# Performance work log

Measured on AMD Instinct MI355X. Metric: run time of the kernel, lower is better.

The kernel has to match this reference:

```python
import jax, jax.numpy as jnp
import numpy as np

D = 256; FF = 1024; NH = 8; NL = 4; NP = 4; DH = D // NH
SHAPES = [(64, 64), (32, 32), (16, 16), (8, 8)]
B = 4; N = sum(h * w for h, w in SHAPES)


def _ln(x, g, b, eps=1e-5):
    m = jnp.mean(x, -1, keepdims=True)
    v = jnp.var(x, -1, keepdims=True)
    return (x - m) * jax.lax.rsqrt(v + eps) * g + b


def _bilinear(v, x, y, H, W):
    # v: [B, H*W, nh, dh]; x, y: [B, Nq, nh, P] pixel coords (grid_sample, align_corners=False, zero pad)
    x0 = jnp.floor(x); y0 = jnp.floor(y)
    fx = x - x0; fy = y - y0
    x0 = x0.astype(jnp.int32); y0 = y0.astype(jnp.int32)
    dh = v.shape[-1]
    acc = 0.0
    for xi, yi, w in ((x0, y0, (1 - fx) * (1 - fy)),
                      (x0 + 1, y0, fx * (1 - fy)),
                      (x0, y0 + 1, (1 - fx) * fy),
                      (x0 + 1, y0 + 1, fx * fy)):
        valid = ((xi >= 0) & (xi < W) & (yi >= 0) & (yi < H)).astype(v.dtype)
        idx = jnp.clip(yi, 0, H - 1) * W + jnp.clip(xi, 0, W - 1)  # [B,Nq,nh,P]
        Bq, Nq, nh, P = idx.shape
        idx2 = idx.transpose(0, 1, 3, 2).reshape(Bq, Nq * P, nh, 1)
        idx2 = jnp.broadcast_to(idx2, (Bq, Nq * P, nh, dh))
        g = jnp.take_along_axis(v, idx2, axis=1)  # [B, Nq*P, nh, dh]
        g = g.reshape(Bq, Nq, P, nh, dh).transpose(0, 1, 3, 2, 4)  # [B,Nq,nh,P,dh]
        acc = acc + g * (w * valid)[..., None]
    return acc


def _msdeform(value, loc, attn, shapes):
    # value [B,N,nh,dh]; loc [B,Nq,nh,L,P,2] in [0,1]; attn [B,Nq,nh,L,P]
    out = 0.0; start = 0
    for l, (H, W) in enumerate(shapes):
        v = value[:, start:start + H * W]
        start += H * W
        x = loc[:, :, :, l, :, 0] * W - 0.5
        y = loc[:, :, :, l, :, 1] * H - 0.5
        s = _bilinear(v, x, y, H, W)  # [B,Nq,nh,P,dh]
        out = out + jnp.einsum('bqhpd,bqhp->bqhd', s, attn[:, :, :, l, :])
    return out


def _forward(src, pos, reference_points, w_value, b_value, w_off, b_off, w_attn, b_attn,
             w_out, b_out, g1, be1, w1, b1, w2, b2, g2, be2, padding_mask, shapes):
    q = src + pos
    value = src @ w_value.T + b_value
    value = jnp.where(padding_mask[..., None], 0.0, value).reshape(B, N, NH, DH)
    off = (q @ w_off.T + b_off).reshape(B, N, NH, NL, NP, 2)
    attn = jax.nn.softmax((q @ w_attn.T + b_attn).reshape(B, N, NH, NL * NP), axis=-1)
    attn = attn.reshape(B, N, NH, NL, NP)
    normalizer = jnp.array([[w, h] for h, w in shapes], jnp.float32)  # [L,2] as (W,H)
    loc = reference_points[:, :, None, :, None, :] + off / normalizer[None, None, None, :, None, :]
    a = _msdeform(value, loc, attn, shapes).reshape(B, N, D) @ w_out.T + b_out
    x = _ln(src + a, g1, be1)
    f = jax.nn.relu(x @ w1.T + b1) @ w2.T + b2
    return _ln(x + f, g2, be2)


def setup_inputs() -> dict:
    key = jax.random.key(0)
    ks = iter(jax.random.split(key, 24))
    def p(shape, scale=0.02):
        return jax.random.normal(next(ks), shape, jnp.float32) * scale
    d = {}
    d['src'] = jax.random.normal(next(ks), (B, N, D), jnp.float32)
    d['pos'] = jax.random.normal(next(ks), (B, N, D), jnp.float32)
    d['reference_points'] = jax.random.uniform(next(ks), (B, N, NL, 2), dtype=jnp.float32)
    d['w_value'] = p((D, D)); d['b_value'] = jnp.zeros((D,), jnp.float32)
    d['w_off'] = p((NH * NL * NP * 2, D), 0.001); d['b_off'] = p((NH * NL * NP * 2,), 0.1)
    d['w_attn'] = p((NH * NL * NP, D)); d['b_attn'] = jnp.zeros((NH * NL * NP,), jnp.float32)
    d['w_out'] = p((D, D)); d['b_out'] = jnp.zeros((D,), jnp.float32)
    d['g1'] = jnp.ones((D,), jnp.float32); d['be1'] = jnp.zeros((D,), jnp.float32)
    d['w1'] = p((FF, D)); d['b1'] = jnp.zeros((FF,), jnp.float32)
    d['w2'] = p((D, FF)); d['b2'] = jnp.zeros((D,), jnp.float32)
    d['g2'] = jnp.ones((D,), jnp.float32); d['be2'] = jnp.zeros((D,), jnp.float32)
    d['spatial_shapes'] = jnp.array(SHAPES, jnp.int32)
    d['level_start_index'] = jnp.array(np.cumsum([0] + [h * w for h, w in SHAPES[:-1]]), jnp.int32)
    d['padding_mask'] = jnp.zeros((B, N), bool)
    return d


def reference(src, pos, reference_points, w_value, b_value, w_off, b_off, w_attn, b_attn,
              w_out, b_out, g1, be1, w1, b1, w2, b2, g2, be2,
              spatial_shapes, level_start_index, padding_mask):
    shapes = [tuple(map(int, s)) for s in np.asarray(spatial_shapes)]  # static per-level shapes
    return _forward(src, pos, reference_points, w_value, b_value, w_off, b_off, w_attn, b_attn,
                    w_out, b_out, g1, be1, w1, b1, w2, b2, g2, be2, padding_mask, shapes)
```

## Files before the change

### kernel.cpp

```cpp
#include <hip/hip_runtime.h>

#define B_SZ   4
#define NTOK   5440
#define MTOT   (B_SZ*NTOK)
#define DMODEL 256
#define FFDIM  1024
#define NROWP  (MTOT/128)

typedef __attribute__((ext_vector_type(8))) __bf16 bf16x8;
typedef __attribute__((ext_vector_type(4))) float  f32x4;

static __device__ __forceinline__ unsigned short f2b(float f) {
    unsigned u = __builtin_bit_cast(unsigned, f);
    u = (u + 0x7FFF + ((u >> 16) & 1)) >> 16;
    return (unsigned short)u;
}
static __device__ __forceinline__ float b2f(unsigned short s) {
    return __builtin_bit_cast(float, (unsigned)s << 16);
}
static __device__ __forceinline__ float lo_bf(unsigned u) {
    return __builtin_bit_cast(float, u << 16);
}
static __device__ __forceinline__ float hi_bf(unsigned u) {
    return __builtin_bit_cast(float, u & 0xffff0000u);
}

#define GLL(gp, lp) __builtin_amdgcn_global_load_lds( \
    (const __attribute__((address_space(1))) void*)(gp), \
    (__attribute__((address_space(3))) void*)(lp), 16, 0, 0)

__global__ __launch_bounds__(256)
void qkv_gemm(const unsigned short* __restrict__ src_bf,
              const unsigned short* __restrict__ q_bf,
              const unsigned short* __restrict__ wv_b,
              const unsigned short* __restrict__ woa_b,
              const float* __restrict__ b_value,
              const float* __restrict__ b_off, const float* __restrict__ b_attn,
              const unsigned char* __restrict__ rowmask,
              unsigned short* __restrict__ value_b, unsigned short* __restrict__ oa_b)
{
    const int K = 256;
    const int id  = blockIdx.x;
    const int xcd = id & 7;
    const int j   = id >> 3;
    const int c   = j % 5;
    const int r   = 8 * (j / 5) + xcd;
    if (r >= NROWP) return;
    const int row0 = r * 128;
    const bool isv = (c < 2);
    const unsigned short* A  = isv ? src_bf : q_bf;
    const unsigned short* Wt = isv ? wv_b : woa_b;
    unsigned short* C = isv ? value_b : oa_b;
    const int ldc  = isv ? 256 : 384;
    const int col0 = (isv ? c : (c - 2)) * 128;

    __shared__ unsigned short As[2][128 * 32];
    __shared__ unsigned short Bs[2][128 * 32];
    const int tid  = threadIdx.x;
    const int lane = tid & 63;
    const int wave = tid >> 6;
    const int wr = (wave >> 1) * 64, wc = (wave & 1) * 64;
    const int mrow = lane & 15, quad = lane >> 4;

    f32x4 acc[4][4] = {};
    const int ri0 = tid >> 2,            ki0 = (tid & 3) * 8;
    const int ri1 = (256 + tid) >> 2,    ki1 = ((256 + tid) & 3) * 8;
    const int lds0 = (wave * 64) * 8, lds1 = (256 + wave * 64) * 8;

    for (int k0 = 0; k0 < K; k0 += 64) {
        __syncthreads();
        #pragma unroll
        for (int s = 0; s < 2; ++s) {
            const int kk = k0 + s * 32;
            GLL(A  + (size_t)(row0 + ri0) * K + kk + ki0, &As[s][lds0]);
            GLL(Wt + (size_t)(col0 + ri0) * K + kk + ki0, &Bs[s][lds0]);
            GLL(A  + (size_t)(row0 + ri1) * K + kk + ki1, &As[s][lds1]);
            GLL(Wt + (size_t)(col0 + ri1) * K + kk + ki1, &Bs[s][lds1]);
        }
        __syncthreads();
        #pragma unroll
        for (int s = 0; s < 2; ++s) {
            bf16x8 af[4], bfr[4];
            #pragma unroll
            for (int t4 = 0; t4 < 4; ++t4) {
                af[t4]  = *(const bf16x8*)&As[s][(wr + t4 * 16 + mrow) * 32 + quad * 8];
                bfr[t4] = *(const bf16x8*)&Bs[s][(wc + t4 * 16 + mrow) * 32 + quad * 8];
            }
            #pragma unroll
            for (int ti = 0; ti < 4; ++ti)
                #pragma unroll
                for (int tj = 0; tj < 4; ++tj)
                    acc[ti][tj] = __builtin_amdgcn_mfma_f32_16x16x32_bf16(
                                      bfr[tj], af[ti], acc[ti][tj], 0, 0, 0);
        }
    }

    #pragma unroll
    for (int ti = 0; ti < 4; ++ti) {
        const int row = row0 + wr + ti * 16 + mrow;
        const bool msk = isv && rowmask[row];
        #pragma unroll
        for (int tj = 0; tj < 4; ++tj) {
            const int col = col0 + wc + tj * 16 + quad * 4;
            const float4 bv = isv ? *(const float4*)(b_value + col)
                            : (col < 256 ? *(const float4*)(b_off + col)
                                         : *(const float4*)(b_attn + col - 256));
            ushort4 o;
            o.x = msk ? 0 : f2b(acc[ti][tj][0] + bv.x);
            o.y = msk ? 0 : f2b(acc[ti][tj][1] + bv.y);
            o.z = msk ? 0 : f2b(acc[ti][tj][2] + bv.z);
            o.w = msk ? 0 : f2b(acc[ti][tj][3] + bv.w);
            *(ushort4*)(C + (size_t)row * ldc + col) = o;
        }
    }
}

__global__ __launch_bounds__(256)
void mfma_gemm(const unsigned short* __restrict__ A,
               const unsigned short* __restrict__ Wt,
               const float* __restrict__ bias,
               unsigned short* __restrict__ Cb,
               int Nout, int K)
{
    const int id  = blockIdx.x;
    const int xcd = id & 7;
    const int j   = id >> 3;
    const int ncol = Nout / 128;
    const int c   = j % ncol;
    const int r   = 8 * (j / ncol) + xcd;
    if (r >= NROWP) return;
    const int row0 = r * 128, col0 = c * 128;

    __shared__ unsigned short As[2][128 * 32];
    __shared__ unsigned short Bs[2][128 * 32];
    const int tid  = threadIdx.x;
    const int lane = tid & 63;
    const int wave = tid >> 6;
    const int wr = (wave >> 1) * 64, wc = (wave & 1) * 64;
    const int mrow = lane & 15, quad = lane >> 4;

    f32x4 acc[4][4] = {};
    const int ri0 = tid >> 2,            ki0 = (tid & 3) * 8;
    const int ri1 = (256 + tid) >> 2,    ki1 = ((256 + tid) & 3) * 8;
    const int lds0 = (wave * 64) * 8, lds1 = (256 + wave * 64) * 8;

    for (int k0 = 0; k0 < K; k0 += 64) {
        __syncthreads();
        #pragma unroll
        for (int s = 0; s < 2; ++s) {
            const int kk = k0 + s * 32;
            GLL(A  + (size_t)(row0 + ri0) * K + kk + ki0, &As[s][lds0]);
            GLL(Wt + (size_t)(col0 + ri0) * K + kk + ki0, &Bs[s][lds0]);
            GLL(A  + (size_t)(row0 + ri1) * K + kk + ki1, &As[s][lds1]);
            GLL(Wt + (size_t)(col0 + ri1) * K + kk + ki1, &Bs[s][lds1]);
        }
        __syncthreads();
        #pragma unroll
        for (int s = 0; s < 2; ++s) {
            bf16x8 af[4], bfr[4];
            #pragma unroll
            for (int t4 = 0; t4 < 4; ++t4) {
                af[t4]  = *(const bf16x8*)&As[s][(wr + t4 * 16 + mrow) * 32 + quad * 8];
                bfr[t4] = *(const bf16x8*)&Bs[s][(wc + t4 * 16 + mrow) * 32 + quad * 8];
            }
            #pragma unroll
            for (int ti = 0; ti < 4; ++ti)
                #pragma unroll
                for (int tj = 0; tj < 4; ++tj)
                    acc[ti][tj] = __builtin_amdgcn_mfma_f32_16x16x32_bf16(
                                      bfr[tj], af[ti], acc[ti][tj], 0, 0, 0);
        }
    }

    #pragma unroll
    for (int ti = 0; ti < 4; ++ti) {
        const int row = row0 + wr + ti * 16 + mrow;
        #pragma unroll
        for (int tj = 0; tj < 4; ++tj) {
            const int col = col0 + wc + tj * 16 + quad * 4;
            const float4 bv = *(const float4*)(bias + col);
            ushort4 o;
            o.x = f2b(fmaxf(acc[ti][tj][0] + bv.x, 0.f));
            o.y = f2b(fmaxf(acc[ti][tj][1] + bv.y, 0.f));
            o.z = f2b(fmaxf(acc[ti][tj][2] + bv.z, 0.f));
            o.w = f2b(fmaxf(acc[ti][tj][3] + bv.w, 0.f));
            *(ushort4*)(Cb + (size_t)row * Nout + col) = o;
        }
    }
}

__global__ __launch_bounds__(256)
void gemm_n64(const unsigned short* __restrict__ A,
              const unsigned short* __restrict__ Wt,
              const float* __restrict__ bias,
              unsigned short* __restrict__ Cb,
              int K)
{
    const int id  = blockIdx.x;
    const int xcd = id & 7;
    const int j   = id >> 3;
    const int c   = j % 4;
    const int r   = 8 * (j / 4) + xcd;
    if (r >= NROWP) return;
    const int row0 = r * 128, col0 = c * 64;

    __shared__ unsigned short As[2][128 * 32];
    __shared__ unsigned short Bs[2][64 * 32];
    const int tid  = threadIdx.x;
    const int lane = tid & 63;
    const int wave = tid >> 6;
    const int wr = wave * 32;
    const int mrow = lane & 15, quad = lane >> 4;

    f32x4 acc[2][4] = {};
    const int ri0 = tid >> 2,            ki0 = (tid & 3) * 8;
    const int ri1 = (256 + tid) >> 2,    ki1 = ((256 + tid) & 3) * 8;
    const int ldsA0 = (wave * 64) * 8, ldsA1 = (256 + wave * 64) * 8;
    const int ldsB  = (wave * 64) * 8;

    for (int k0 = 0; k0 < K; k0 += 64) {
        __syncthreads();
        #pragma unroll
        for (int s = 0; s < 2; ++s) {
            const int kk = k0 + s * 32;
            GLL(A  + (size_t)(row0 + ri0) * K + kk + ki0, &As[s][ldsA0]);
            GLL(A  + (size_t)(row0 + ri1) * K + kk + ki1, &As[s][ldsA1]);
            GLL(Wt + (size_t)(col0 + ri0) * K + kk + ki0, &Bs[s][ldsB]);
        }
        __syncthreads();
        #pragma unroll
        for (int s = 0; s < 2; ++s) {
            bf16x8 af[2], bfr[4];
            #pragma unroll
            for (int ti = 0; ti < 2; ++ti)
                af[ti] = *(const bf16x8*)&As[s][(wr + ti * 16 + mrow) * 32 + quad * 8];
            #pragma unroll
            for (int tj = 0; tj < 4; ++tj)
                bfr[tj] = *(const bf16x8*)&Bs[s][(tj * 16 + mrow) * 32 + quad * 8];
            #pragma unroll
            for (int ti = 0; ti < 2; ++ti)
                #pragma unroll
                for (int tj = 0; tj < 4; ++tj)
                    acc[ti][tj] = __builtin_amdgcn_mfma_f32_16x16x32_bf16(
                                      bfr[tj], af[ti], acc[ti][tj], 0, 0, 0);
        }
    }

    #pragma unroll
    for (int ti = 0; ti < 2; ++ti) {
        const int row = row0 + wr + ti * 16 + mrow;
        #pragma unroll
        for (int tj = 0; tj < 4; ++tj) {
            const int col = col0 + tj * 16 + quad * 4;
            const float4 bv = *(const float4*)(bias + col);
            ushort4 o;
            o.x = f2b(acc[ti][tj][0] + bv.x);
            o.y = f2b(acc[ti][tj][1] + bv.y);
            o.z = f2b(acc[ti][tj][2] + bv.z);
            o.w = f2b(acc[ti][tj][3] + bv.w);
            *(ushort4*)(Cb + (size_t)row * 256 + col) = o;
        }
    }
}

__global__ __launch_bounds__(256)
void addln_kernel(const unsigned short* __restrict__ c,
                  const float* __restrict__ resid_f,
                  const unsigned short* __restrict__ resid_b,
                  const float* __restrict__ g, const float* __restrict__ be,
                  float* __restrict__ out_f, unsigned short* __restrict__ out_b)
{
    const int wave = threadIdx.x >> 6;
    const int lane = threadIdx.x & 63;
    const int row  = blockIdx.x * 4 + wave;
    const size_t base = (size_t)row * 256 + (lane << 2);

    const ushort4 cu = *(const ushort4*)(c + base);
    float4 v;
    v.x = b2f(cu.x); v.y = b2f(cu.y); v.z = b2f(cu.z); v.w = b2f(cu.w);
    if (resid_f) {
        const float4 r = *(const float4*)(resid_f + base);
        v.x += r.x; v.y += r.y; v.z += r.z; v.w += r.w;
    } else {
        const ushort4 r = *(const ushort4*)(resid_b + base);
        v.x += b2f(r.x); v.y += b2f(r.y); v.z += b2f(r.z); v.w += b2f(r.w);
    }

    float s  = v.x + v.y + v.z + v.w;
    float ss = v.x * v.x + v.y * v.y + v.z * v.z + v.w * v.w;
    #pragma unroll
    for (int off = 32; off; off >>= 1) {
        s  += __shfl_xor(s, off, 64);
        ss += __shfl_xor(ss, off, 64);
    }
    const float mean = s * (1.f / 256.f);
    const float var  = ss * (1.f / 256.f) - mean * mean;
    const float rstd = rsqrtf(var + 1e-5f);

    const float4 gv = *(const float4*)(g  + (lane << 2));
    const float4 bv = *(const float4*)(be + (lane << 2));
    float4 o;
    o.x = (v.x - mean) * rstd * gv.x + bv.x;
    o.y = (v.y - mean) * rstd * gv.y + bv.y;
    o.z = (v.z - mean) * rstd * gv.z + bv.z;
    o.w = (v.w - mean) * rstd * gv.w + bv.w;
    if (out_f) *(float4*)(out_f + base) = o;
    if (out_b) {
        ushort4 u; u.x = f2b(o.x); u.y = f2b(o.y); u.z = f2b(o.z); u.w = f2b(o.w);
        *(ushort4*)(out_b + base) = u;
    }
}

__global__ __launch_bounds__(256)
void sampling_kernel(const unsigned short* __restrict__ value,
                     const unsigned short* __restrict__ oa,
                     const float* __restrict__ refp,
                     unsigned short* __restrict__ samp)
{
    __shared__ unsigned s_pk[64 * 68];
    const int t0  = blockIdx.x * 8;
    const int tid = threadIdx.x;

    #pragma unroll
    for (int rep = 0; rep < 4; ++rep) {
        const int e   = rep * 256 + tid;
        const int tok = e >> 7;
        const int hp  = e & 127;
        const int h   = hp >> 4, i16 = hp & 15, l = i16 >> 2;
        const int t   = t0 + tok;

        const float ex = __expf(b2f(oa[(size_t)t * 384 + 256 + h * 16 + i16]));
        float ssum = ex;
        #pragma unroll
        for (int o = 8; o; o >>= 1) ssum += __shfl_xor(ssum, o, 16);
        const float aw = ex / ssum;

        const int   Wl_t[4]  = {64, 32, 16, 8};
        const int   LST_t[4] = {0, 4096, 5120, 5376};
        const int   Wl  = Wl_t[l];
        const int   LST = LST_t[l];
        const float fW  = (float)Wl;

        const unsigned ov = *(const unsigned*)&oa[(size_t)t * 384 + h * 32 + i16 * 2];
        const float ox = lo_bf(ov), oy = hi_bf(ov);
        const float2 rxy = *(const float2*)&refp[(size_t)t * 8 + l * 2];
        const float x = rxy.x * fW + ox - 0.5f;
        const float y = rxy.y * fW + oy - 0.5f;
        const float x0 = floorf(x), y0 = floorf(y);
        const float fx = x - x0, fy = y - y0;
        const int   ix = (int)x0, iy = (int)y0;
        const bool  vx0 = (ix >= 0) & (ix < Wl), vx1 = (ix + 1 >= 0) & (ix + 1 < Wl);

        const int base = (tok * 8 + h) * 68 + i16 * 4;
        #pragma unroll
        for (int j = 0; j < 2; ++j) {
            const int  yv = iy + j;
            const bool vy = (yv >= 0) & (yv < Wl);
            const float wy = (j ? fy : 1.f - fy) * aw;
            const int  rowi = LST + yv * Wl;
            const float w0 = (vy & vx0) ? wy * (1.f - fx) : 0.f;
            const float w1 = (vy & vx1) ? wy * fx : 0.f;
            const unsigned i0 = (vy & vx0) ? (unsigned)(rowi + ix) : 0u;
            const unsigned i1 = (vy & vx1) ? (unsigned)(rowi + ix + 1) : 0u;
            s_pk[base + j * 2 + 0] = (i0 << 16) | f2b(w0);
            s_pk[base + j * 2 + 1] = (i1 << 16) | f2b(w1);
        }
    }
    __syncthreads();

    const int wv_  = tid >> 6;
    const int lane = tid & 63;
    const int t2   = lane >> 5;
    const int h    = (lane >> 2) & 7;
    const int dq   = lane & 3;
    const int tok  = wv_ * 2 + t2;
    const int t    = t0 + tok;
    const int b    = t / NTOK;
    const char* vb = (const char*)value + ((size_t)b * NTOK * 256 + h * 32 + dq * 8) * 2;
    const unsigned* sp = s_pk + (tok * 8 + h) * 68;

    float a0 = 0.f, a1 = 0.f, a2 = 0.f, a3 = 0.f;
    float a4 = 0.f, a5 = 0.f, a6 = 0.f, a7 = 0.f;

    unsigned pkc = sp[0];
    uint4 vc = *(const uint4*)(vb + (size_t)(pkc >> 16) * 512);
    #pragma unroll 8
    for (int i = 0; i < 64; ++i) {
        unsigned pkn = 0; uint4 vn = make_uint4(0, 0, 0, 0);
        if (i < 63) {
            pkn = sp[i + 1];
            vn = *(const uint4*)(vb + (size_t)(pkn >> 16) * 512);
        }
        const float w = lo_bf(pkc);
        a0 += lo_bf(vc.x) * w; a1 += hi_bf(vc.x) * w;
        a2 += lo_bf(vc.y) * w; a3 += hi_bf(vc.y) * w;
        a4 += lo_bf(vc.z) * w; a5 += hi_bf(vc.z) * w;
        a6 += lo_bf(vc.w) * w; a7 += hi_bf(vc.w) * w;
        pkc = pkn; vc = vn;
    }
    ushort4 o0, o1;
    o0.x = f2b(a0); o0.y = f2b(a1); o0.z = f2b(a2); o0.w = f2b(a3);
    o1.x = f2b(a4); o1.y = f2b(a5); o1.z = f2b(a6); o1.w = f2b(a7);
    unsigned short* op = samp + (size_t)t * 256 + h * 32 + dq * 8;
    *(ushort4*)(op)     = o0;
    *(ushort4*)(op + 4) = o1;
}

__global__ __launch_bounds__(256)
void prep_kernel(const float* __restrict__ src, const float* __restrict__ pos,
                 const float* __restrict__ wv, const float* __restrict__ woff,
                 const float* __restrict__ wattn, const float* __restrict__ wout,
                 const float* __restrict__ w1, const float* __restrict__ w2,
                 unsigned short* __restrict__ q_bf, unsigned short* __restrict__ src_bf,
                 unsigned short* __restrict__ wv_b, unsigned short* __restrict__ woa_b,
                 unsigned short* __restrict__ wout_b,
                 unsigned short* __restrict__ w1_b, unsigned short* __restrict__ w2_b)
{
    const int v = blockIdx.x * 256 + threadIdx.x;
    if (v < 1392640) {
        const float4 s = ((const float4*)src)[v];
        const float4 p = ((const float4*)pos)[v];
        ushort4 qo, so;
        qo.x = f2b(s.x + p.x); qo.y = f2b(s.y + p.y);
        qo.z = f2b(s.z + p.z); qo.w = f2b(s.w + p.w);
        so.x = f2b(s.x); so.y = f2b(s.y); so.z = f2b(s.z); so.w = f2b(s.w);
        ((ushort4*)q_bf)[v]   = qo;
        ((ushort4*)src_bf)[v] = so;
        return;
    }
    const int v2 = v - 1392640;
    const float* s; unsigned short* d; int off;
    if      (v2 <  16384) { s = wv;    d = wv_b;          off = v2; }
    else if (v2 <  32768) { s = woff;  d = woa_b;         off = v2 - 16384; }
    else if (v2 <  40960) { s = wattn; d = woa_b + 65536; off = v2 - 32768; }
    else if (v2 <  57344) { s = wout;  d = wout_b;        off = v2 - 40960; }
    else if (v2 < 122880) { s = w1;    d = w1_b;          off = v2 - 57344; }
    else                  { s = w2;    d = w2_b;          off = v2 - 122880; }
    const float4 f = ((const float4*)s)[off];
    ushort4 u; u.x = f2b(f.x); u.y = f2b(f.y); u.z = f2b(f.z); u.w = f2b(f.w);
    ((ushort4*)d)[off] = u;
}

extern "C" void kernel_launch(void* const* d_in, const int* in_sizes, int n_in,
                              void* d_out, int out_size, void* d_ws, size_t ws_size,
                              hipStream_t stream) {
    const float* src     = (const float*)d_in[0];
    const float* pos     = (const float*)d_in[1];
    const float* refp    = (const float*)d_in[2];
    const float* w_value = (const float*)d_in[3];
    const float* b_value = (const float*)d_in[4];
    const float* w_off   = (const float*)d_in[5];
    const float* b_off   = (const float*)d_in[6];
    const float* w_attn  = (const float*)d_in[7];
    const float* b_attn  = (const float*)d_in[8];
    const float* w_out   = (const float*)d_in[9];
    const float* b_out   = (const float*)d_in[10];
    const float* g1      = (const float*)d_in[11];
    const float* be1     = (const float*)d_in[12];
    const float* w1      = (const float*)d_in[13];
    const float* b1      = (const float*)d_in[14];
    const float* w2      = (const float*)d_in[15];
    const float* b2      = (const float*)d_in[16];
    const float* g2      = (const float*)d_in[17];
    const float* be2     = (const float*)d_in[18];
    const unsigned char* pmask = (const unsigned char*)d_in[21];

    char* ws = (char*)d_ws;
    const size_t SZ16 = (size_t)MTOT * 256 * 2;
    unsigned short* q_bf    = (unsigned short*)(ws);
    unsigned short* src_bf  = (unsigned short*)(ws + SZ16);
    unsigned short* value_b = (unsigned short*)(ws + 2 * SZ16);
    unsigned short* oa_b    = (unsigned short*)(ws + 3 * SZ16);
    unsigned short* samp    = (unsigned short*)(ws + 3 * SZ16 + SZ16 * 3 / 2);
    unsigned short* h_bf    = (unsigned short*)(ws + 5 * SZ16 + SZ16 * 3 / 2);
    unsigned short* wts     = (unsigned short*)(ws + 9 * SZ16 + SZ16 * 3 / 2);
    unsigned short* C1_bf   = (unsigned short*)(ws + 2 * SZ16);
    unsigned short* x_bf    = (unsigned short*)(ws);
    unsigned short* C2_bf   = samp;

    unsigned short* wv_b    = wts;
    unsigned short* woa_b   = wv_b   + 65536;
    unsigned short* wout_b  = woa_b  + 98304;
    unsigned short* w1_b    = wout_b + 65536;
    unsigned short* w2_b    = w1_b   + 262144;

    const dim3 blk(256);

    prep_kernel<<<dim3(6176), blk, 0, stream>>>(src, pos, w_value, w_off, w_attn,
                                                w_out, w1, w2, q_bf, src_bf,
                                                wv_b, woa_b, wout_b, w1_b, w2_b);
    qkv_gemm<<<dim3(8 * 5 * 22), blk, 0, stream>>>(
        src_bf, q_bf, wv_b, woa_b, b_value, b_off, b_attn, pmask, value_b, oa_b);
    sampling_kernel<<<dim3(MTOT / 8), blk, 0, stream>>>(value_b, oa_b, refp, samp);
    gemm_n64<<<dim3(8 * 4 * 22), blk, 0, stream>>>(
        samp, wout_b, b_out, C1_bf, DMODEL);
    addln_kernel<<<dim3(MTOT / 4), blk, 0, stream>>>(
        C1_bf, src, nullptr, g1, be1, nullptr, x_bf);
    mfma_gemm<<<dim3(8 * 8 * 22), blk, 0, stream>>>(
        x_bf, w1_b, b1, h_bf, FFDIM, DMODEL);
    gemm_n64<<<dim3(8 * 4 * 22), blk, 0, stream>>>(
        h_bf, w2_b, b2, C2_bf, FFDIM);
    addln_kernel<<<dim3(MTOT / 4), blk, 0, stream>>>(
        C2_bf, nullptr, x_bf, g2, be2, (float*)d_out, nullptr);
}
```

Measured before the change: 273.7 us.

## Software-pipeline GEMM K-loops with explicit waitcnts and batch sampling gathers

The three GEMM kernels now prefetch the next 32-wide K slice into the free LDS buffer while MFMAs run on the current one. Raw s_waitcnt and s_barrier calls replace the paired __syncthreads, and K is made a compile-time constant so the loops fully unroll. The sampling kernel issues eight independent value gathers before accumulating them, which raises memory-level parallelism at the cost of more registers. The workspace buffers are also remapped, which risks aliasing mistakes if the fixed offsets overlap live data.

```diff
diff --git a/kernel.cpp b/kernel.cpp
--- a/kernel.cpp
+++ b/kernel.cpp
@@ -28,6 +28,10 @@
 #define GLL(gp, lp) __builtin_amdgcn_global_load_lds( \
     (const __attribute__((address_space(1))) void*)(gp), \
     (__attribute__((address_space(3))) void*)(lp), 16, 0, 0)
+
+#define WAITVM(n)  __builtin_amdgcn_s_waitcnt(0x0F70 | (n))
+#define WAITLGKM0  __builtin_amdgcn_s_waitcnt(0xC07F)
+#define BAR        __builtin_amdgcn_s_barrier()
 
 __global__ __launch_bounds__(256)
 void qkv_gemm(const unsigned short* __restrict__ src_bf,
@@ -62,37 +66,46 @@
     const int wr = (wave >> 1) * 64, wc = (wave & 1) * 64;
     const int mrow = lane & 15, quad = lane >> 4;
 
+    const int ri0 = tid >> 2,         ki0 = (tid & 3) * 8;
+    const int ri1 = (256 + tid) >> 2, ki1 = ((256 + tid) & 3) * 8;
+    const int lds0 = (wave * 64) * 8, lds1 = (256 + wave * 64) * 8;
+
+    const unsigned short* Ar0 = A  + (size_t)(row0 + ri0) * K + ki0;
+    const unsigned short* Br0 = Wt + (size_t)(col0 + ri0) * K + ki0;
+    const unsigned short* Ar1 = A  + (size_t)(row0 + ri1) * K + ki1;
+    const unsigned short* Br1 = Wt + (size_t)(col0 + ri1) * K + ki1;
+
     f32x4 acc[4][4] = {};
-    const int ri0 = tid >> 2,            ki0 = (tid & 3) * 8;
-    const int ri1 = (256 + tid) >> 2,    ki1 = ((256 + tid) & 3) * 8;
-    const int lds0 = (wave * 64) * 8, lds1 = (256 + wave * 64) * 8;
-
-    for (int k0 = 0; k0 < K; k0 += 64) {
-        __syncthreads();
-        #pragma unroll
-        for (int s = 0; s < 2; ++s) {
-            const int kk = k0 + s * 32;
-            GLL(A  + (size_t)(row0 + ri0) * K + kk + ki0, &As[s][lds0]);
-            GLL(Wt + (size_t)(col0 + ri0) * K + kk + ki0, &Bs[s][lds0]);
-            GLL(A  + (size_t)(row0 + ri1) * K + kk + ki1, &As[s][lds1]);
-            GLL(Wt + (size_t)(col0 + ri1) * K + kk + ki1, &Bs[s][lds1]);
-        }
-        __syncthreads();
-        #pragma unroll
-        for (int s = 0; s < 2; ++s) {
-            bf16x8 af[4], bfr[4];
+
+    GLL(Ar0 +  0, &As[0][lds0]); GLL(Br0 +  0, &Bs[0][lds0]);
+    GLL(Ar1 +  0, &As[0][lds1]); GLL(Br1 +  0, &Bs[0][lds1]);
+    GLL(Ar0 + 32, &As[1][lds0]); GLL(Br0 + 32, &Bs[1][lds0]);
+    GLL(Ar1 + 32, &As[1][lds1]); GLL(Br1 + 32, &Bs[1][lds1]);
+
+    #pragma unroll
+    for (int k = 0; k < 8; ++k) {
+        if (k < 7) WAITVM(4); else WAITVM(0);
+        BAR;
+        const int b = k & 1;
+        bf16x8 af[4], bfr[4];
+        #pragma unroll
+        for (int t4 = 0; t4 < 4; ++t4) {
+            af[t4]  = *(const bf16x8*)&As[b][(wr + t4 * 16 + mrow) * 32 + quad * 8];
+            bfr[t4] = *(const bf16x8*)&Bs[b][(wc + t4 * 16 + mrow) * 32 + quad * 8];
+        }
+        WAITLGKM0;
+        BAR;
+        if (k + 2 < 8) {
+            const int kk = (k + 2) * 32;
+            GLL(Ar0 + kk, &As[b][lds0]); GLL(Br0 + kk, &Bs[b][lds0]);
+            GLL(Ar1 + kk, &As[b][lds1]); GLL(Br1 + kk, &Bs[b][lds1]);
+        }
+        #pragma unroll
+        for (int ti = 0; ti < 4; ++ti)
             #pragma unroll
-            for (int t4 = 0; t4 < 4; ++t4) {
-                af[t4]  = *(const bf16x8*)&As[s][(wr + t4 * 16 + mrow) * 32 + quad * 8];
-                bfr[t4] = *(const bf16x8*)&Bs[s][(wc + t4 * 16 + mrow) * 32 + quad * 8];
-            }
-            #pragma unroll
-            for (int ti = 0; ti < 4; ++ti)
-                #pragma unroll
-                for (int tj = 0; tj < 4; ++tj)
-                    acc[ti][tj] = __builtin_amdgcn_mfma_f32_16x16x32_bf16(
-                                      bfr[tj], af[ti], acc[ti][tj], 0, 0, 0);
-        }
+            for (int tj = 0; tj < 4; ++tj)
+                acc[ti][tj] = __builtin_amdgcn_mfma_f32_16x16x32_bf16(
+                                  bfr[tj], af[ti], acc[ti][tj], 0, 0, 0);
     }
 
     #pragma unroll
@@ -116,18 +129,17 @@
 }
 
 __global__ __launch_bounds__(256)
-void mfma_gemm(const unsigned short* __restrict__ A,
+void ffn1_gemm(const unsigned short* __restrict__ A,
                const unsigned short* __restrict__ Wt,
                const float* __restrict__ bias,
-               unsigned short* __restrict__ Cb,
-               int Nout, int K)
+               unsigned short* __restrict__ Cb)
 {
+    const int K = 256, Nout = 1024;
     const int id  = blockIdx.x;
     const int xcd = id & 7;
     const int j   = id >> 3;
-    const int ncol = Nout / 128;
-    const int c   = j % ncol;
-    const int r   = 8 * (j / ncol) + xcd;
+    const int c   = j & 7;
+    const int r   = 8 * (j >> 3) + xcd;
     if (r >= NROWP) return;
     const int row0 = r * 128, col0 = c * 128;
 
@@ -139,37 +151,46 @@
     const int wr = (wave >> 1) * 64, wc = (wave & 1) * 64;
     const int mrow = lane & 15, quad = lane >> 4;
 
+    const int ri0 = tid >> 2,         ki0 = (tid & 3) * 8;
+    const int ri1 = (256 + tid) >> 2, ki1 = ((256 + tid) & 3) * 8;
+    const int lds0 = (wave * 64) * 8, lds1 = (256 + wave * 64) * 8;
+
+    const unsigned short* Ar0 = A  + (size_t)(row0 + ri0) * K + ki0;
+    const unsigned short* Br0 = Wt + (size_t)(col0 + ri0) * K + ki0;
+    const unsigned short* Ar1 = A  + (size_t)(row0 + ri1) * K + ki1;
+    const unsigned short* Br1 = Wt + (size_t)(col0 + ri1) * K + ki1;
+
     f32x4 acc[4][4] = {};
-    const int ri0 = tid >> 2,            ki0 = (tid & 3) * 8;
-    const int ri1 = (256 + tid) >> 2,    ki1 = ((256 + tid) & 3) * 8;
-    const int lds0 = (wave * 64) * 8, lds1 = (256 + wave * 64) * 8;
-
-    for (int k0 = 0; k0 < K; k0 += 64) {
-        __syncthreads();
-        #pragma unroll
-        for (int s = 0; s < 2; ++s) {
-            const int kk = k0 + s * 32;
-            GLL(A  + (size_t)(row0 + ri0) * K + kk + ki0, &As[s][lds0]);
-            GLL(Wt + (size_t)(col0 + ri0) * K + kk + ki0, &Bs[s][lds0]);
-            GLL(A  + (size_t)(row0 + ri1) * K + kk + ki1, &As[s][lds1]);
-            GLL(Wt + (size_t)(col0 + ri1) * K + kk + ki1, &Bs[s][lds1]);
-        }
-        __syncthreads();
-        #pragma unroll
-        for (int s = 0; s < 2; ++s) {
-            bf16x8 af[4], bfr[4];
+
+    GLL(Ar0 +  0, &As[0][lds0]); GLL(Br0 +  0, &Bs[0][lds0]);
+    GLL(Ar1 +  0, &As[0][lds1]); GLL(Br1 +  0, &Bs[0][lds1]);
+    GLL(Ar0 + 32, &As[1][lds0]); GLL(Br0 + 32, &Bs[1][lds0]);
+    GLL(Ar1 + 32, &As[1][lds1]); GLL(Br1 + 32, &Bs[1][lds1]);
+
+    #pragma unroll
+    for (int k = 0; k < 8; ++k) {
+        if (k < 7) WAITVM(4); else WAITVM(0);
+        BAR;
+        const int b = k & 1;
+        bf16x8 af[4], bfr[4];
+        #pragma unroll
+        for (int t4 = 0; t4 < 4; ++t4) {
+            af[t4]  = *(const bf16x8*)&As[b][(wr + t4 * 16 + mrow) * 32 + quad * 8];
+            bfr[t4] = *(const bf16x8*)&Bs[b][(wc + t4 * 16 + mrow) * 32 + quad * 8];
+        }
+        WAITLGKM0;
+        BAR;
+        if (k + 2 < 8) {
+            const int kk = (k + 2) * 32;
+            GLL(Ar0 + kk, &As[b][lds0]); GLL(Br0 + kk, &Bs[b][lds0]);
+            GLL(Ar1 + kk, &As[b][lds1]); GLL(Br1 + kk, &Bs[b][lds1]);
+        }
+        #pragma unroll
+        for (int ti = 0; ti < 4; ++ti)
             #pragma unroll
-            for (int t4 = 0; t4 < 4; ++t4) {
-                af[t4]  = *(const bf16x8*)&As[s][(wr + t4 * 16 + mrow) * 32 + quad * 8];
-                bfr[t4] = *(const bf16x8*)&Bs[s][(wc + t4 * 16 + mrow) * 32 + quad * 8];
-            }
-            #pragma unroll
-            for (int ti = 0; ti < 4; ++ti)
-                #pragma unroll
-                for (int tj = 0; tj < 4; ++tj)
-                    acc[ti][tj] = __builtin_amdgcn_mfma_f32_16x16x32_bf16(
-                                      bfr[tj], af[ti], acc[ti][tj], 0, 0, 0);
-        }
+            for (int tj = 0; tj < 4; ++tj)
+                acc[ti][tj] = __builtin_amdgcn_mfma_f32_16x16x32_bf16(
+                                  bfr[tj], af[ti], acc[ti][tj], 0, 0, 0);
     }
 
     #pragma unroll
@@ -189,18 +210,19 @@
     }
 }
 
+template<int NK>
 __global__ __launch_bounds__(256)
 void gemm_n64(const unsigned short* __restrict__ A,
               const unsigned short* __restrict__ Wt,
               const float* __restrict__ bias,
-              unsigned short* __restrict__ Cb,
-              int K)
+              unsigned short* __restrict__ Cb)
 {
+    const int K = NK * 32;
     const int id  = blockIdx.x;
     const int xcd = id & 7;
     const int j   = id >> 3;
-    const int c   = j % 4;
-    const int r   = 8 * (j / 4) + xcd;
+    const int c   = j & 3;
+    const int r   = 8 * (j >> 2) + xcd;
     if (r >= NROWP) return;
     const int row0 = r * 128, col0 = c * 64;
 
@@ -212,38 +234,46 @@
     const int wr = wave * 32;
     const int mrow = lane & 15, quad = lane >> 4;
 
+    const int ri0 = tid >> 2,         ki0 = (tid & 3) * 8;
+    const int ri1 = (256 + tid) >> 2, ki1 = ((256 + tid) & 3) * 8;
+    const int lds0 = (wave * 64) * 8, lds1 = (256 + wave * 64) * 8;
+
+    const unsigned short* Ar0 = A  + (size_t)(row0 + ri0) * K + ki0;
+    const unsigned short* Ar1 = A  + (size_t)(row0 + ri1) * K + ki1;
+    const unsigned short* Br0 = Wt + (size_t)(col0 + ri0) * K + ki0;
+
     f32x4 acc[2][4] = {};
-    const int ri0 = tid >> 2,            ki0 = (tid & 3) * 8;
-    const int ri1 = (256 + tid) >> 2,    ki1 = ((256 + tid) & 3) * 8;
-    const int ldsA0 = (wave * 64) * 8, ldsA1 = (256 + wave * 64) * 8;
-    const int ldsB  = (wave * 64) * 8;
-
-    for (int k0 = 0; k0 < K; k0 += 64) {
-        __syncthreads();
-        #pragma unroll
-        for (int s = 0; s < 2; ++s) {
-            const int kk = k0 + s * 32;
-            GLL(A  + (size_t)(row0 + ri0) * K + kk + ki0, &As[s][ldsA0]);
-            GLL(A  + (size_t)(row0 + ri1) * K + kk + ki1, &As[s][ldsA1]);
-            GLL(Wt + (size_t)(col0 + ri0) * K + kk + ki0, &Bs[s][ldsB]);
-        }
-        __syncthreads();
-        #pragma unroll
-        for (int s = 0; s < 2; ++s) {
-            bf16x8 af[2], bfr[4];
-            #pragma unroll
-            for (int ti = 0; ti < 2; ++ti)
-                af[ti] = *(const bf16x8*)&As[s][(wr + ti * 16 + mrow) * 32 + quad * 8];
+
+    GLL(Ar0 +  0, &As[0][lds0]); GLL(Ar1 +  0, &As[0][lds1]);
+    GLL(Br0 +  0, &Bs[0][lds0]);
+    GLL(Ar0 + 32, &As[1][lds0]); GLL(Ar1 + 32, &As[1][lds1]);
+    GLL(Br0 + 32, &Bs[1][lds0]);
+
+    #pragma unroll
+    for (int k = 0; k < NK; ++k) {
+        if (k < NK - 1) WAITVM(3); else WAITVM(0);
+        BAR;
+        const int b = k & 1;
+        bf16x8 af[2], bfr[4];
+        #pragma unroll
+        for (int ti = 0; ti < 2; ++ti)
+            af[ti] = *(const bf16x8*)&As[b][(wr + ti * 16 + mrow) * 32 + quad * 8];
+        #pragma unroll
+        for (int tj = 0; tj < 4; ++tj)
+            bfr[tj] = *(const bf16x8*)&Bs[b][(tj * 16 + mrow) * 32 + quad * 8];
+        WAITLGKM0;
+        BAR;
+        if (k + 2 < NK) {
+            const int kk = (k + 2) * 32;
+            GLL(Ar0 + kk, &As[b][lds0]); GLL(Ar1 + kk, &As[b][lds1]);
+            GLL(Br0 + kk, &Bs[b][lds0]);
+        }
+        #pragma unroll
+        for (int ti = 0; ti < 2; ++ti)
             #pragma unroll
             for (int tj = 0; tj < 4; ++tj)
-                bfr[tj] = *(const bf16x8*)&Bs[s][(tj * 16 + mrow) * 32 + quad * 8];
-            #pragma unroll
-            for (int ti = 0; ti < 2; ++ti)
-                #pragma unroll
-                for (int tj = 0; tj < 4; ++tj)
-                    acc[ti][tj] = __builtin_amdgcn_mfma_f32_16x16x32_bf16(
-                                      bfr[tj], af[ti], acc[ti][tj], 0, 0, 0);
-        }
+                acc[ti][tj] = __builtin_amdgcn_mfma_f32_16x16x32_bf16(
+                                  bfr[tj], af[ti], acc[ti][tj], 0, 0, 0);
     }
 
     #pragma unroll
@@ -353,17 +383,17 @@
 
         const int base = (tok * 8 + h) * 68 + i16 * 4;
         #pragma unroll
-        for (int j = 0; j < 2; ++j) {
-            const int  yv = iy + j;
+        for (int jj = 0; jj < 2; ++jj) {
+            const int  yv = iy + jj;
             const bool vy = (yv >= 0) & (yv < Wl);
-            const float wy = (j ? fy : 1.f - fy) * aw;
+            const float wy = (jj ? fy : 1.f - fy) * aw;
             const int  rowi = LST + yv * Wl;
             const float w0 = (vy & vx0) ? wy * (1.f - fx) : 0.f;
             const float w1 = (vy & vx1) ? wy * fx : 0.f;
             const unsigned i0 = (vy & vx0) ? (unsigned)(rowi + ix) : 0u;
             const unsigned i1 = (vy & vx1) ? (unsigned)(rowi + ix + 1) : 0u;
-            s_pk[base + j * 2 + 0] = (i0 << 16) | f2b(w0);
-            s_pk[base + j * 2 + 1] = (i1 << 16) | f2b(w1);
+            s_pk[base + jj * 2 + 0] = (i0 << 16) | f2b(w0);
+            s_pk[base + jj * 2 + 1] = (i1 << 16) | f2b(w1);
         }
     }
     __syncthreads();
@@ -382,21 +412,23 @@
     float a0 = 0.f, a1 = 0.f, a2 = 0.f, a3 = 0.f;
     float a4 = 0.f, a5 = 0.f, a6 = 0.f, a7 = 0.f;
 
-    unsigned pkc = sp[0];
-    uint4 vc = *(const uint4*)(vb + (size_t)(pkc >> 16) * 512);
-    #pragma unroll 8
-    for (int i = 0; i < 64; ++i) {
-        unsigned pkn = 0; uint4 vn = make_uint4(0, 0, 0, 0);
-        if (i < 63) {
-            pkn = sp[i + 1];
-            vn = *(const uint4*)(vb + (size_t)(pkn >> 16) * 512);
-        }
-        const float w = lo_bf(pkc);
-        a0 += lo_bf(vc.x) * w; a1 += hi_bf(vc.x) * w;
-        a2 += lo_bf(vc.y) * w; a3 += hi_bf(vc.y) * w;
-        a4 += lo_bf(vc.z) * w; a5 += hi_bf(vc.z) * w;
-        a6 += lo_bf(vc.w) * w; a7 += hi_bf(vc.w) * w;
-        pkc = pkn; vc = vn;
+    #pragma unroll
+    for (int g = 0; g < 8; ++g) {
+        unsigned pk[8];
+        #pragma unroll
+        for (int jj = 0; jj < 8; ++jj) pk[jj] = sp[g * 8 + jj];
+        uint4 vv[8];
+        #pragma unroll
+        for (int jj = 0; jj < 8; ++jj)
+            vv[jj] = *(const uint4*)(vb + (size_t)(pk[jj] >> 16) * 512);
+        #pragma unroll
+        for (int jj = 0; jj < 8; ++jj) {
+            const float w = lo_bf(pk[jj]);
+            a0 += lo_bf(vv[jj].x) * w; a1 += hi_bf(vv[jj].x) * w;
+            a2 += lo_bf(vv[jj].y) * w; a3 += hi_bf(vv[jj].y) * w;
+            a4 += lo_bf(vv[jj].z) * w; a5 += hi_bf(vv[jj].z) * w;
+            a6 += lo_bf(vv[jj].w) * w; a7 += hi_bf(vv[jj].w) * w;
+        }
     }
     ushort4 o0, o1;
     o0.x = f2b(a0); o0.y = f2b(a1); o0.z = f2b(a2); o0.w = f2b(a3);
@@ -471,12 +503,12 @@
     unsigned short* src_bf  = (unsigned short*)(ws + SZ16);
     unsigned short* value_b = (unsigned short*)(ws + 2 * SZ16);
     unsigned short* oa_b    = (unsigned short*)(ws + 3 * SZ16);
-    unsigned short* samp    = (unsigned short*)(ws + 3 * SZ16 + SZ16 * 3 / 2);
-    unsigned short* h_bf    = (unsigned short*)(ws + 5 * SZ16 + SZ16 * 3 / 2);
-    unsigned short* wts     = (unsigned short*)(ws + 9 * SZ16 + SZ16 * 3 / 2);
-    unsigned short* C1_bf   = (unsigned short*)(ws + 2 * SZ16);
-    unsigned short* x_bf    = (unsigned short*)(ws);
-    unsigned short* C2_bf   = samp;
+    unsigned short* samp    = (unsigned short*)(ws + 50135040ULL);
+    unsigned short* h_bf    = (unsigned short*)(ws + 3 * SZ16);
+    unsigned short* wts     = (unsigned short*)(ws + 77987840ULL);
+    unsigned short* x_bf    = q_bf;
+    unsigned short* C1_bf   = value_b;
+    unsigned short* C2_bf   = src_bf;
 
     unsigned short* wv_b    = wts;
     unsigned short* woa_b   = wv_b   + 65536;
@@ -492,14 +524,11 @@
     qkv_gemm<<<dim3(8 * 5 * 22), blk, 0, stream>>>(
         src_bf, q_bf, wv_b, woa_b, b_value, b_off, b_attn, pmask, value_b, oa_b);
     sampling_kernel<<<dim3(MTOT / 8), blk, 0, stream>>>(value_b, oa_b, refp, samp);
-    gemm_n64<<<dim3(8 * 4 * 22), blk, 0, stream>>>(
-        samp, wout_b, b_out, C1_bf, DMODEL);
+    gemm_n64<8><<<dim3(8 * 4 * 22), blk, 0, stream>>>(samp, wout_b, b_out, C1_bf);
     addln_kernel<<<dim3(MTOT / 4), blk, 0, stream>>>(
         C1_bf, src, nullptr, g1, be1, nullptr, x_bf);
-    mfma_gemm<<<dim3(8 * 8 * 22), blk, 0, stream>>>(
-        x_bf, w1_b, b1, h_bf, FFDIM, DMODEL);
-    gemm_n64<<<dim3(8 * 4 * 22), blk, 0, stream>>>(
-        h_bf, w2_b, b2, C2_bf, FFDIM);
+    ffn1_gemm<<<dim3(8 * 8 * 22), blk, 0, stream>>>(x_bf, w1_b, b1, h_bf);
+    gemm_n64<32><<<dim3(8 * 4 * 22), blk, 0, stream>>>(h_bf, w2_b, b2, C2_bf);
     addln_kernel<<<dim3(MTOT / 4), blk, 0, stream>>>(
         C2_bf, nullptr, x_bf, g2, be2, (float*)d_out, nullptr);
 }
```

New measurement: 270.2 us. Within noise of the previous version (-1.3%).
